# Performance work log

Measured on AMD Instinct MI355X. Metric: run time of the kernel, lower is better.

The kernel has to match this reference:

```python
import jax, jax.numpy as jnp
import numpy as np

B, C, H, W = 32, 3, 512, 512
PCT = 3.0  # normalization_percentile_threshold
D0 = int(max(0.5 * min(H, W) // 2, 1))  # = 128


def _build_filter_map():
    # cv2.rectangle(thickness=-1) fills inclusive of both corner points, clipped to image
    f = np.zeros((H, W), dtype=np.float32)
    f[:D0 + 1, :D0 + 1] = 1.0
    f[:D0 + 1, W - D0:] = 1.0
    f[H - D0:, :D0 + 1] = 1.0
    f[H - D0:, W - D0:] = 1.0
    return jnp.asarray(f)


def setup_inputs() -> dict:
    key = jax.random.key(0)
    k1, k2 = jax.random.split(key)
    x = jax.random.normal(k1, (B, C, H, W), dtype=jnp.float32)
    # binary field-of-view mask, broadcastable over channels
    mask = (jax.random.uniform(k2, (B, 1, H, W)) > 0.2).astype(jnp.float32)
    return {"x": x, "mask": mask, "filter_map": _build_filter_map()}


def _median_padding(x, mask):
    b, c, h, w = x.shape
    # torch.median returns the LOWER of the two middle values for even counts
    flat = x.reshape(b, c, h * w)
    med = jnp.sort(flat, axis=-1)[..., (h * w - 1) // 2] + 0.2  # [B, C]
    med = med[:, :, None, None]
    return mask * x + (1.0 - mask) * med


def reference(x, mask, filter_map):
    x = _median_padding(x, mask)
    # FFT2 over last two dims, corner-keep frequency mask, magnitude of ifft2
    res = jnp.abs(jnp.fft.ifft2(jnp.fft.fft2(x) * filter_map))
    b, c, h, w = res.shape
    # quantize as (res*256).int().float()/256  -> truncation toward zero
    q = jnp.trunc(res * 256.0) / 256.0
    qf = q.reshape(b, c, h * w)
    lo = jnp.percentile(qf, PCT, axis=-1)          # [B, C]
    hi = jnp.percentile(qf, 100.0 - PCT, axis=-1)  # [B, C]
    res = (res - lo[:, :, None, None]) / (hi - lo)[:, :, None, None]
    return res * mask  # sub_mask=True
```

## Files before the change

### kernel.cpp

```cpp
#include <hip/hip_runtime.h>
#include <math.h>

#define HW 262144
#define NIMG 96
#define NQBIN 4096

typedef __attribute__((ext_vector_type(8))) short bf16x8;
typedef __attribute__((ext_vector_type(4))) float f32x4;

__device__ __forceinline__ unsigned fmap_u(float f){
  unsigned u = __float_as_uint(f);
  return (u & 0x80000000u) ? ~u : (u | 0x80000000u);
}
__device__ __forceinline__ float funmap_u(unsigned u){
  unsigned v = (u & 0x80000000u) ? (u & 0x7fffffffu) : ~u;
  return __uint_as_float(v);
}
__device__ __forceinline__ unsigned bf16rne(float f){
  unsigned u = __float_as_uint(f);
  return (u + 0x7fffu + ((u >> 16) & 1u)) >> 16;
}

typedef __attribute__((address_space(3))) unsigned lds_u;
typedef const __attribute__((address_space(1))) unsigned glb_u;
__device__ __forceinline__ void gll16(const void* g, void* l){
  __builtin_amdgcn_global_load_lds((glb_u*)g, (lds_u*)l, 16, 0, 0);
}

__global__ void k_dir(const float* __restrict__ fmap_in, float* __restrict__ Dir){
  int n = blockIdx.x;
  int t = threadIdx.x;
  double s = 0.0;
  for(int c = t; c < 512; c += 256){
    int a = (c * n) & 511;
    s += (double)fmap_in[c] * cos(6.283185307179586476925287 * (double)a / 512.0);
  }
  __shared__ double red[256];
  red[t] = s; __syncthreads();
  for(int off = 128; off; off >>= 1){
    if(t < off) red[t] += red[t + off];
    __syncthreads();
  }
  if(t == 0) Dir[n] = (float)(red[0] / 512.0);
}

__global__ void k_cmat(const float* __restrict__ Dir, unsigned short* __restrict__ CmH,
                       unsigned* __restrict__ h1){
  int a = blockIdx.x;
  for(int b = threadIdx.x; b < 512; b += 256){
    float d = Dir[(a - b) & 511];
    CmH[(size_t)a * 512 + b] = (unsigned short)bf16rne(d);
  }
  unsigned idx = blockIdx.x * 256 + threadIdx.x;
  #pragma unroll
  for(int j = 0; j < 3; j++) h1[idx + j * 131072u] = 0;
}

__global__ __launch_bounds__(256) void k_p1(const float* __restrict__ x, unsigned* __restrict__ h){
  __shared__ unsigned sh[2][4112];
  const int img  = blockIdx.x >> 3;
  const int part = blockIdx.x & 7;
  const int par  = threadIdx.x & 1;
  const float4* p = (const float4*)(x + (size_t)img * HW + (size_t)part * 32768);
  for(int i = threadIdx.x; i < 4112; i += 256){ sh[0][i] = 0; sh[1][i] = 0; }
  __syncthreads();
  unsigned* mine = sh[par];
  for(int i = threadIdx.x; i < 8192; i += 256){
    float4 v = p[i];
    atomicAdd(&mine[fmap_u(v.x) >> 20], 1u);
    atomicAdd(&mine[fmap_u(v.y) >> 20], 1u);
    atomicAdd(&mine[fmap_u(v.z) >> 20], 1u);
    atomicAdd(&mine[fmap_u(v.w) >> 20], 1u);
  }
  __syncthreads();
  unsigned* hh = h + (size_t)img * 4096;
  for(int i = threadIdx.x; i < 4096; i += 256){
    unsigned c = sh[0][i] + sh[1][i];
    if(c) atomicAdd(&hh[i], c);
  }
}

__global__ void k_med12(const unsigned* __restrict__ h, float* __restrict__ med){
  int img = blockIdx.x, t = threadIdx.x;
  const unsigned* hh = h + (size_t)img * 4096;
  __shared__ unsigned csum[256];
  unsigned s = 0;
  for(int j = 0; j < 16; j++) s += hh[t * 16 + j];
  csum[t] = s; __syncthreads();
  if(t == 0){
    unsigned k = 131071u, cum = 0; int chunk = 0;
    for(; chunk < 256; ++chunk){ if(cum + csum[chunk] > k) break; cum += csum[chunk]; }
    int b = chunk * 16;
    unsigned c;
    for(;; ++b){ c = hh[b]; if(cum + c > k) break; cum += c; }
    float frac = ((float)(k - cum) + 0.5f) / (float)c;
    unsigned m = ((unsigned)b << 20) + (unsigned)(frac * 1048576.0f);
    med[img] = funmap_u(m) + 0.2f;
  }
}

__global__ __launch_bounds__(256) void k_prepad(
    const float* __restrict__ x, const float* __restrict__ mask,
    const float* __restrict__ med, unsigned short* __restrict__ xh,
    unsigned* __restrict__ qh)
{
  size_t u8 = (size_t)blockIdx.x * 256 + threadIdx.x;
  if(u8 < (size_t)NIMG * NQBIN) qh[u8] = 0;
  size_t i  = u8 * 8;
  int img = (int)(i >> 18);
  size_t mi = ((size_t)(img / 3) << 18) + (i & 0x3FFFFu);
  const float mv = med[img];
  unsigned hp[4];
  #pragma unroll
  for(int q = 0; q < 2; q++){
    float4 xv = *(const float4*)(x + i + q * 4);
    float4 mk = *(const float4*)(mask + mi + q * 4);
    unsigned h0 = bf16rne((mk.x != 0.f) ? xv.x : mv);
    unsigned h1 = bf16rne((mk.y != 0.f) ? xv.y : mv);
    unsigned h2 = bf16rne((mk.z != 0.f) ? xv.z : mv);
    unsigned h3 = bf16rne((mk.w != 0.f) ? xv.w : mv);
    hp[q*2]   = (h1 << 16) | h0;
    hp[q*2+1] = (h3 << 16) | h2;
  }
  *(uint4*)(xh + i) = make_uint4(hp[0], hp[1], hp[2], hp[3]);
}

__global__ __launch_bounds__(512, 6) void k_rowpass(
    const unsigned short* __restrict__ xh,
    const unsigned short* __restrict__ CmH,
    unsigned short* __restrict__ t1h)
{
  __shared__ __align__(16) unsigned short As [2][4096];
  __shared__ __align__(16) unsigned short BsH[2][4096];

  const int b    = blockIdx.x;
  const int xcd  = b & 7;
  const int i8   = b >> 3;
  const int rblk = xcd * 48 + (i8 >> 2);
  const int nblk = i8 & 3;
  const int r0 = rblk * 128;
  const int n0 = nblk * 128;

  const int t    = threadIdx.x;
  const int lane = t & 63;
  const int wv   = t >> 6;
  const int wm   = (wv >> 2) * 64;
  const int wn   = (wv & 3) * 32;
  const int fr   = lane & 15;
  const int fg   = lane >> 4;
  const int co   = ((fg ^ (fr & 3)) << 3);

  const int drow = lane >> 2;
  const int dblk = (lane & 3) ^ (drow & 3);
  const unsigned short* asrc  = xh  + ((size_t)(r0 + wv*16 + drow) << 9) + dblk * 8;
  const unsigned short* bhsrc = CmH + ((size_t)(n0 + wv*16 + drow) << 9) + dblk * 8;
  const int dbase = wv * 512;

  f32x4 acc[4][2];
  #pragma unroll
  for(int i = 0; i < 4; i++)
    #pragma unroll
    for(int j = 0; j < 2; j++) acc[i][j] = (f32x4){0.f, 0.f, 0.f, 0.f};

  auto STAGE = [&](int buf, int k0){
    gll16(asrc  + k0, &As [buf][dbase]);
    gll16(bhsrc + k0, &BsH[buf][dbase]);
  };
  auto COMPUTE = [&](int buf){
    bf16x8 af[4], bh[2];
    #pragma unroll
    for(int i = 0; i < 4; i++)
      af[i] = *(const bf16x8*)&As[buf][(wm + i*16 + fr) * 32 + co];
    #pragma unroll
    for(int j = 0; j < 2; j++)
      bh[j] = *(const bf16x8*)&BsH[buf][(wn + j*16 + fr) * 32 + co];
    __builtin_amdgcn_s_setprio(1);
    #pragma unroll
    for(int i = 0; i < 4; i++)
      #pragma unroll
      for(int j = 0; j < 2; j++)
        acc[i][j] = __builtin_amdgcn_mfma_f32_16x16x32_bf16(af[i], bh[j], acc[i][j], 0, 0, 0);
    __builtin_amdgcn_s_setprio(0);
  };

  STAGE(0, 0);
  asm volatile("s_waitcnt vmcnt(0)" ::: "memory");
  __builtin_amdgcn_s_barrier();
  #pragma unroll
  for(int it = 0; it < 15; ++it){
    STAGE((it + 1) & 1, (it + 1) * 32);
    asm volatile("s_waitcnt vmcnt(2)" ::: "memory");
    __builtin_amdgcn_s_barrier();
    COMPUTE(it & 1);
    asm volatile("" ::: "memory");
    __builtin_amdgcn_s_barrier();
  }
  asm volatile("s_waitcnt vmcnt(0)" ::: "memory");
  __builtin_amdgcn_s_barrier();
  COMPUTE(1);

  const int img = r0 >> 9;
  const int hb  = r0 & 511;
  #pragma unroll
  for(int i = 0; i < 4; i++)
    #pragma unroll
    for(int j = 0; j < 2; j++){
      f32x4 a = acc[i][j];
      unsigned b0 = bf16rne(a[0]), b1 = bf16rne(a[1]), b2 = bf16rne(a[2]), b3 = bf16rne(a[3]);
      int n = n0 + wn + j*16 + fr;
      int h = hb + wm + i*16 + fg*4;
      *(uint2*)&t1h[(size_t)img * HW + ((size_t)n << 9) + h] =
          make_uint2((b1<<16)|b0, (b3<<16)|b2);
    }
}

__global__ __launch_bounds__(512, 6) void k_colpass(
    const unsigned short* __restrict__ t1h,
    const unsigned short* __restrict__ CmH,
    unsigned short* __restrict__ resh, unsigned* __restrict__ qh)
{
  __shared__ __align__(16) unsigned short AsH[2][4096];
  __shared__ __align__(16) unsigned short Bs [2][4096];

  const int b    = blockIdx.x;
  const int xcd  = b & 7;
  const int i8   = b >> 3;
  const int img  = xcd * 12 + (i8 >> 4);
  const int r16  = i8 & 15;
  const int hp0  = (r16 >> 2) * 128;
  const int w0   = (r16 & 3) * 128;

  const int t    = threadIdx.x;
  const int lane = t & 63;
  const int wv   = t >> 6;
  const int wm   = (wv >> 2) * 64;
  const int wn   = (wv & 3) * 32;
  const int fr   = lane & 15;
  const int fg   = lane >> 4;
  const int co   = ((fg ^ (fr & 3)) << 3);

  const int drow = lane >> 2;
  const int dblk = (lane & 3) ^ (drow & 3);
  const unsigned short* ahsrc = CmH + ((size_t)(hp0 + wv*16 + drow) << 9) + dblk * 8;
  const unsigned short* bsrc  = t1h + (size_t)img * HW + ((size_t)(w0 + wv*16 + drow) << 9) + dblk * 8;
  const int dbase = wv * 512;

  f32x4 acc[4][2];
  #pragma unroll
  for(int i = 0; i < 4; i++)
    #pragma unroll
    for(int j = 0; j < 2; j++) acc[i][j] = (f32x4){0.f, 0.f, 0.f, 0.f};

  auto STAGE = [&](int buf, int k0){
    gll16(ahsrc + k0, &AsH[buf][dbase]);
    gll16(bsrc  + k0, &Bs [buf][dbase]);
  };
  auto COMPUTE = [&](int buf){
    bf16x8 ah[4], bv[2];
    #pragma unroll
    for(int i = 0; i < 4; i++)
      ah[i] = *(const bf16x8*)&AsH[buf][(wm + i*16 + fr) * 32 + co];
    #pragma unroll
    for(int j = 0; j < 2; j++)
      bv[j] = *(const bf16x8*)&Bs[buf][(wn + j*16 + fr) * 32 + co];
    __builtin_amdgcn_s_setprio(1);
    #pragma unroll
    for(int i = 0; i < 4; i++)
      #pragma unroll
      for(int j = 0; j < 2; j++)
        acc[i][j] = __builtin_amdgcn_mfma_f32_16x16x32_bf16(ah[i], bv[j], acc[i][j], 0, 0, 0);
    __builtin_amdgcn_s_setprio(0);
  };

  STAGE(0, 0);
  asm volatile("s_waitcnt vmcnt(0)" ::: "memory");
  __builtin_amdgcn_s_barrier();
  #pragma unroll
  for(int it = 0; it < 15; ++it){
    STAGE((it + 1) & 1, (it + 1) * 32);
    asm volatile("s_waitcnt vmcnt(2)" ::: "memory");
    __builtin_amdgcn_s_barrier();
    COMPUTE(it & 1);
    asm volatile("" ::: "memory");
    __builtin_amdgcn_s_barrier();
  }
  asm volatile("s_waitcnt vmcnt(0)" ::: "memory");
  __builtin_amdgcn_s_barrier();
  COMPUTE(1);

  __syncthreads();
  unsigned* shh = (unsigned*)&AsH[0][0];
  for(int i = t; i < NQBIN; i += 512) shh[i] = 0;
  __syncthreads();

  unsigned short* rimg = resh + (size_t)img * HW;
  #pragma unroll
  for(int i = 0; i < 4; i++)
    #pragma unroll
    for(int j = 0; j < 2; j++){
      f32x4 a = acc[i][j];
      int w  = w0 + wn + j*16 + fr;
      int hp = hp0 + wm + i*16 + fg*4;
      #pragma unroll
      for(int r = 0; r < 4; r++){
        float v = fabsf(a[r]);
        rimg[((size_t)(hp + r) << 9) + w] = (unsigned short)bf16rne(v);
        atomicAdd(&shh[min((int)(v * 256.f), NQBIN - 1)], 1u);
      }
    }
  __syncthreads();

  unsigned* hg = qh + (size_t)img * NQBIN;
  for(int i = t; i < NQBIN; i += 512){
    unsigned c = shh[i];
    if(c) atomicAdd(&hg[i], c);
  }
}

__global__ void k_pct(const unsigned* __restrict__ qh, float2* __restrict__ prm){
  int img = blockIdx.x, t = threadIdx.x;
  const unsigned* h = qh + (size_t)img * NQBIN;
  __shared__ unsigned sh[NQBIN];
  for(int i = t; i < NQBIN; i += 256) sh[i] = h[i];
  __syncthreads();
  if(t == 0){
    const unsigned targ[4] = {7864u, 7865u, 254278u, 254279u};
    float v[4]; unsigned cum = 0; int b = 0;
    for(int q = 0; q < 4; q++){
      while(cum + sh[b] <= targ[q]){ cum += sh[b]; ++b; }
      v[q] = (float)b * (1.0f / 256.0f);
    }
    double plo = 0.03 * 262143.0;
    double phi = 0.97 * 262143.0;
    float lo = v[0] + (float)(plo - 7864.0)   * (v[1] - v[0]);
    float hi = v[2] + (float)(phi - 254278.0) * (v[3] - v[2]);
    prm[img] = make_float2(lo, 1.0f / (hi - lo));
  }
}

__global__ __launch_bounds__(256) void k_norm(const unsigned short* __restrict__ resh,
                                              const float* __restrict__ mask,
                                              const float2* __restrict__ prm,
                                              float* __restrict__ out){
  size_t i8 = (size_t)blockIdx.x * blockDim.x + threadIdx.x;
  const size_t total8 = (size_t)NIMG * HW / 8;
  const size_t step = (size_t)gridDim.x * blockDim.x;
  for(; i8 < total8; i8 += step){
    size_t i = i8 * 8;
    int bc = (int)(i >> 18);
    int bb = bc / 3;
    size_t mi = ((size_t)bb << 18) + (i & 0x3FFFFu);
    uint4 rv = *(const uint4*)(resh + i);
    float4 m0 = *(const float4*)(mask + mi);
    float4 m1 = *(const float4*)(mask + mi + 4);
    float2 p = prm[bc];
    float4 o0, o1;
    o0.x = (__uint_as_float((rv.x & 0xFFFFu) << 16) - p.x) * p.y * m0.x;
    o0.y = (__uint_as_float((rv.x & 0xFFFF0000u))   - p.x) * p.y * m0.y;
    o0.z = (__uint_as_float((rv.y & 0xFFFFu) << 16) - p.x) * p.y * m0.z;
    o0.w = (__uint_as_float((rv.y & 0xFFFF0000u))   - p.x) * p.y * m0.w;
    o1.x = (__uint_as_float((rv.z & 0xFFFFu) << 16) - p.x) * p.y * m1.x;
    o1.y = (__uint_as_float((rv.z & 0xFFFF0000u))   - p.x) * p.y * m1.y;
    o1.z = (__uint_as_float((rv.w & 0xFFFFu) << 16) - p.x) * p.y * m1.z;
    o1.w = (__uint_as_float((rv.w & 0xFFFF0000u))   - p.x) * p.y * m1.w;
    *(float4*)(out + i)     = o0;
    *(float4*)(out + i + 4) = o1;
  }
}

extern "C" void kernel_launch(void* const* d_in, const int* in_sizes, int n_in,
                              void* d_out, int out_size, void* d_ws, size_t ws_size,
                              hipStream_t stream)
{
  const float* x       = (const float*)d_in[0];
  const float* mask    = (const float*)d_in[1];
  const float* fmap_in = (const float*)d_in[2];
  float* out = (float*)d_out;

  const size_t T1_BYTES = (size_t)NIMG * HW * 2;
  const size_t QH_BYTES = (size_t)NIMG * NQBIN * 4;
  char* ws = (char*)d_ws;
  unsigned short* t1h  = (unsigned short*)ws;
  unsigned*       qh   = (unsigned*)(ws + T1_BYTES);
  unsigned short* xh   = (unsigned short*)(ws + T1_BYTES + QH_BYTES);
  unsigned short* resh = xh;
  unsigned* h1 = (unsigned*)ws;
  char* tail = ws + 2 * T1_BYTES + QH_BYTES;
  float*          Dir = (float*)tail;
  unsigned short* CmH = (unsigned short*)(tail + 2048);
  char* tail2 = tail + 2048 + 524288;
  float*  med  = (float*)tail2;
  float2* prm  = (float2*)(tail2 + 512);

  k_dir<<<512, 256, 0, stream>>>(fmap_in, Dir);
  k_cmat<<<512, 256, 0, stream>>>(Dir, CmH, h1);

  k_p1<<<NIMG * 8, 256, 0, stream>>>(x, h1);
  k_med12<<<NIMG, 256, 0, stream>>>(h1, med);

  k_prepad<<<(NIMG * HW / 8) / 256, 256, 0, stream>>>(x, mask, med, xh, qh);

  k_rowpass<<<1536, 512, 0, stream>>>(xh, CmH, t1h);
  k_colpass<<<1536, 512, 0, stream>>>(t1h, CmH, resh, qh);

  k_pct<<<NIMG, 256, 0, stream>>>(qh, prm);
  k_norm<<<2048, 256, 0, stream>>>(resh, mask, prm, out);
}
```

Baseline: 198.5 us.

## Triple-buffer GEMM LDS staging and change swizzle to rotate-by-row-pair

Both the row-pass and column-pass DFT GEMM kernels go from double-buffered to triple-buffered LDS staging, keeping two global-to-LDS loads in flight ahead of compute. The LDS swizzle also changes from an XOR pattern to a rotation keyed on row>>1, applied the same way to the load offsets and the fragment reads, to reduce bank conflicts. The extra buffer raises LDS use per block from 32KB to 48KB, which may lower the number of resident blocks per CU given launch_bounds(512,6).

```diff
diff --git a/kernel.cpp b/kernel.cpp
--- a/kernel.cpp
+++ b/kernel.cpp
@@ -130,8 +130,8 @@
     const unsigned short* __restrict__ CmH,
     unsigned short* __restrict__ t1h)
 {
-  __shared__ __align__(16) unsigned short As [2][4096];
-  __shared__ __align__(16) unsigned short BsH[2][4096];
+  __shared__ __align__(16) unsigned short As [3][4096];
+  __shared__ __align__(16) unsigned short BsH[3][4096];
 
   const int b    = blockIdx.x;
   const int xcd  = b & 7;
@@ -148,12 +148,12 @@
   const int wn   = (wv & 3) * 32;
   const int fr   = lane & 15;
   const int fg   = lane >> 4;
-  const int co   = ((fg ^ (fr & 3)) << 3);
 
   const int drow = lane >> 2;
-  const int dblk = (lane & 3) ^ (drow & 3);
-  const unsigned short* asrc  = xh  + ((size_t)(r0 + wv*16 + drow) << 9) + dblk * 8;
-  const unsigned short* bhsrc = CmH + ((size_t)(n0 + wv*16 + drow) << 9) + dblk * 8;
+  const int grow = wv * 16 + drow;
+  const int dblk = ((lane & 3) - (grow >> 1)) & 3;
+  const unsigned short* asrc  = xh  + ((size_t)(r0 + grow) << 9) + dblk * 8;
+  const unsigned short* bhsrc = CmH + ((size_t)(n0 + grow) << 9) + dblk * 8;
   const int dbase = wv * 512;
 
   f32x4 acc[4][2];
@@ -169,11 +169,15 @@
   auto COMPUTE = [&](int buf){
     bf16x8 af[4], bh[2];
     #pragma unroll
-    for(int i = 0; i < 4; i++)
-      af[i] = *(const bf16x8*)&As[buf][(wm + i*16 + fr) * 32 + co];
-    #pragma unroll
-    for(int j = 0; j < 2; j++)
-      bh[j] = *(const bf16x8*)&BsH[buf][(wn + j*16 + fr) * 32 + co];
+    for(int i = 0; i < 4; i++){
+      int row = wm + i*16 + fr;
+      af[i] = *(const bf16x8*)&As[buf][row*32 + ((((row>>1) + fg) & 3) << 3)];
+    }
+    #pragma unroll
+    for(int j = 0; j < 2; j++){
+      int row = wn + j*16 + fr;
+      bh[j] = *(const bf16x8*)&BsH[buf][row*32 + ((((row>>1) + fg) & 3) << 3)];
+    }
     __builtin_amdgcn_s_setprio(1);
     #pragma unroll
     for(int i = 0; i < 4; i++)
@@ -183,21 +187,26 @@
     __builtin_amdgcn_s_setprio(0);
   };
 
-  STAGE(0, 0);
-  asm volatile("s_waitcnt vmcnt(0)" ::: "memory");
-  __builtin_amdgcn_s_barrier();
-  #pragma unroll
-  for(int it = 0; it < 15; ++it){
-    STAGE((it + 1) & 1, (it + 1) * 32);
-    asm volatile("s_waitcnt vmcnt(2)" ::: "memory");
+  STAGE(0, 0); STAGE(1, 32);
+  asm volatile("s_waitcnt vmcnt(2)" ::: "memory");
+  __builtin_amdgcn_s_barrier();
+  #pragma unroll
+  for(int it = 0; it < 14; ++it){
+    STAGE((it + 2) % 3, (it + 2) * 32);
+    asm volatile("s_waitcnt vmcnt(4)" ::: "memory");
     __builtin_amdgcn_s_barrier();
-    COMPUTE(it & 1);
+    COMPUTE(it % 3);
     asm volatile("" ::: "memory");
     __builtin_amdgcn_s_barrier();
   }
+  asm volatile("s_waitcnt vmcnt(2)" ::: "memory");
+  __builtin_amdgcn_s_barrier();
+  COMPUTE(14 % 3);
+  asm volatile("" ::: "memory");
+  __builtin_amdgcn_s_barrier();
   asm volatile("s_waitcnt vmcnt(0)" ::: "memory");
   __builtin_amdgcn_s_barrier();
-  COMPUTE(1);
+  COMPUTE(15 % 3);
 
   const int img = r0 >> 9;
   const int hb  = r0 & 511;
@@ -219,8 +228,8 @@
     const unsigned short* __restrict__ CmH,
     unsigned short* __restrict__ resh, unsigned* __restrict__ qh)
 {
-  __shared__ __align__(16) unsigned short AsH[2][4096];
-  __shared__ __align__(16) unsigned short Bs [2][4096];
+  __shared__ __align__(16) unsigned short AsH[3][4096];
+  __shared__ __align__(16) unsigned short Bs [3][4096];
 
   const int b    = blockIdx.x;
   const int xcd  = b & 7;
@@ -237,12 +246,12 @@
   const int wn   = (wv & 3) * 32;
   const int fr   = lane & 15;
   const int fg   = lane >> 4;
-  const int co   = ((fg ^ (fr & 3)) << 3);
 
   const int drow = lane >> 2;
-  const int dblk = (lane & 3) ^ (drow & 3);
-  const unsigned short* ahsrc = CmH + ((size_t)(hp0 + wv*16 + drow) << 9) + dblk * 8;
-  const unsigned short* bsrc  = t1h + (size_t)img * HW + ((size_t)(w0 + wv*16 + drow) << 9) + dblk * 8;
+  const int grow = wv * 16 + drow;
+  const int dblk = ((lane & 3) - (grow >> 1)) & 3;
+  const unsigned short* ahsrc = CmH + ((size_t)(hp0 + grow) << 9) + dblk * 8;
+  const unsigned short* bsrc  = t1h + (size_t)img * HW + ((size_t)(w0 + grow) << 9) + dblk * 8;
   const int dbase = wv * 512;
 
   f32x4 acc[4][2];
@@ -258,11 +267,15 @@
   auto COMPUTE = [&](int buf){
     bf16x8 ah[4], bv[2];
     #pragma unroll
-    for(int i = 0; i < 4; i++)
-      ah[i] = *(const bf16x8*)&AsH[buf][(wm + i*16 + fr) * 32 + co];
-    #pragma unroll
-    for(int j = 0; j < 2; j++)
-      bv[j] = *(const bf16x8*)&Bs[buf][(wn + j*16 + fr) * 32 + co];
+    for(int i = 0; i < 4; i++){
+      int row = wm + i*16 + fr;
+      ah[i] = *(const bf16x8*)&AsH[buf][row*32 + ((((row>>1) + fg) & 3) << 3)];
+    }
+    #pragma unroll
+    for(int j = 0; j < 2; j++){
+      int row = wn + j*16 + fr;
+      bv[j] = *(const bf16x8*)&Bs[buf][row*32 + ((((row>>1) + fg) & 3) << 3)];
+    }
     __builtin_amdgcn_s_setprio(1);
     #pragma unroll
     for(int i = 0; i < 4; i++)
@@ -272,21 +285,26 @@
     __builtin_amdgcn_s_setprio(0);
   };
 
-  STAGE(0, 0);
-  asm volatile("s_waitcnt vmcnt(0)" ::: "memory");
-  __builtin_amdgcn_s_barrier();
-  #pragma unroll
-  for(int it = 0; it < 15; ++it){
-    STAGE((it + 1) & 1, (it + 1) * 32);
-    asm volatile("s_waitcnt vmcnt(2)" ::: "memory");
+  STAGE(0, 0); STAGE(1, 32);
+  asm volatile("s_waitcnt vmcnt(2)" ::: "memory");
+  __builtin_amdgcn_s_barrier();
+  #pragma unroll
+  for(int it = 0; it < 14; ++it){
+    STAGE((it + 2) % 3, (it + 2) * 32);
+    asm volatile("s_waitcnt vmcnt(4)" ::: "memory");
     __builtin_amdgcn_s_barrier();
-    COMPUTE(it & 1);
+    COMPUTE(it % 3);
     asm volatile("" ::: "memory");
     __builtin_amdgcn_s_barrier();
   }
+  asm volatile("s_waitcnt vmcnt(2)" ::: "memory");
+  __builtin_amdgcn_s_barrier();
+  COMPUTE(14 % 3);
+  asm volatile("" ::: "memory");
+  __builtin_amdgcn_s_barrier();
   asm volatile("s_waitcnt vmcnt(0)" ::: "memory");
   __builtin_amdgcn_s_barrier();
-  COMPUTE(1);
+  COMPUTE(15 % 3);
 
   __syncthreads();
   unsigned* shh = (unsigned*)&AsH[0][0];
```

Result: faster. 194.4 us (-2.1%).
